# Kernel tuning notes

Measured on AMD Instinct MI355X. Metric: run time of the kernel, lower is better.

Reference implementation:

```python
import jax, jax.numpy as jnp
import numpy as np

DEGREE = 5
A = 1.0
B = 1.0
IN_F = 1024
OUT_F = 1024
BATCH = 8192


def setup_inputs() -> dict:
    key = jax.random.key(0)
    k1, k2, k3, k4 = jax.random.split(key, 4)
    x = jax.random.normal(k1, (BATCH, IN_F), dtype=jnp.float32)
    # base_weight ~ kaiming-uniform-ish scale
    bound_w = 1.0 / np.sqrt(IN_F)
    base_weight = jax.random.uniform(k2, (OUT_F, IN_F), dtype=jnp.float32,
                                     minval=-bound_w, maxval=bound_w)
    std = 1.0 / (IN_F * np.sqrt(DEGREE + 1))
    jacobi_coeffs = std * jax.random.normal(k3, (OUT_F, IN_F, DEGREE + 1), dtype=jnp.float32)
    bias = jax.random.uniform(k4, (OUT_F,), dtype=jnp.float32, minval=-bound_w, maxval=bound_w)
    return {"x": x, "base_weight": base_weight, "jacobi_coeffs": jacobi_coeffs, "bias": bias}


def _jacobi_polynomials(x):
    # x: (batch, in_features) -> (batch, in_features, DEGREE+1)
    t = jnp.tanh(x)
    polys = [jnp.ones_like(t)]
    if DEGREE >= 1:
        polys.append(0.5 * (2.0 * (A + 1.0) * t + (A - B)))
    for k in range(2, DEGREE + 1):
        # recurrence coefficients (matching torch loop where k = written index)
        alpha_n = 2.0 * k * (k + A + B) * (2 * k + A + B - 2)
        beta_n = (2 * k + A + B - 1) * (A ** 2 - B ** 2)
        gamma_n = (2 * k + A + B - 2) * (2 * k + A + B - 1) * (2 * k + A + B)
        delta_n = 2.0 * (k + A - 1) * (k + B - 1) * (2 * k + A + B)
        Acoef = (beta_n + alpha_n * t) / gamma_n
        Bcoef = delta_n / gamma_n
        polys.append(Acoef * polys[k - 1] - Bcoef * polys[k - 2])
    return jnp.stack(polys, axis=-1)


def reference(x, base_weight, jacobi_coeffs, bias):
    # base branch: SiLU then linear
    base_out = jax.nn.silu(x) @ base_weight.T  # (b, out)
    # jacobi branch
    P = _jacobi_polynomials(x)  # (b, in, deg+1)
    jac_out = jnp.einsum('bik,oik->bo', P, jacobi_coeffs)
    return base_out + jac_out + bias
```

## Files before the change

### kernel.cpp

```cpp
#include <hip/hip_runtime.h>
#include <hip/hip_bf16.h>
#include <cstdint>
#include <cstddef>

#define BATCH   8192
#define IN_F    1024
#define OUT_F   1024
#define KAUG    (6 * 1024)

typedef __bf16 bf16x8 __attribute__((ext_vector_type(8)));
typedef float  f32x4  __attribute__((ext_vector_type(4)));

static constexpr size_t WAUG_B    = (size_t)OUT_F * KAUG * 2;
static constexpr size_t BIAS2_OFF = WAUG_B;
static constexpr size_t AAUG_OFF  = WAUG_B + 4096;
static constexpr size_t AAUG_B    = (size_t)BATCH * KAUG * 2;
static constexpr size_t MMAP_OFF  = AAUG_OFF + AAUG_B;
static constexpr size_t NMAP_OFF  = MMAP_OFF + 1024;

__device__ __constant__ float JAC_A[4] = {64.f/120.f, 180.f/336.f, 384.f/720.f, 700.f/1320.f};
__device__ __constant__ float JAC_B[4] = {48.f/120.f, 144.f/336.f, 320.f/720.f, 600.f/1320.f};

__device__ __forceinline__ unsigned short f2bf(float f)
{
    __hip_bfloat16 h = __float2bfloat16(f);
    return *(unsigned short*)&h;
}
__device__ __forceinline__ unsigned pack2(float lo, float hi)
{
    return (unsigned)f2bf(lo) | ((unsigned)f2bf(hi) << 16);
}
__device__ __forceinline__ float fast_tanh(float x)
{
    const float xc = fminf(fmaxf(x, -15.f), 15.f);
    const float e  = __expf(2.f * xc);
    return (e - 1.f) / (e + 1.f);
}

__global__ void probe_layout(int* __restrict__ mmap, int* __restrict__ nmap)
{
    __shared__ __align__(16) __hip_bfloat16 A1[16 * 32], B1[16 * 32];
    __shared__ __align__(16) __hip_bfloat16 A2[16 * 32], B2[16 * 32];
    const int lane = threadIdx.x;
    for (int e = lane; e < 512; e += 64) {
        const int m = e >> 5, k = e & 31;
        A1[e] = __float2bfloat16((k == 0) ? (float)(m + 1) : 0.f);
        B1[e] = __float2bfloat16((k == 0) ? 1.f : 0.f);
        A2[e] = __float2bfloat16((k == 0) ? 1.f : 0.f);
        B2[e] = __float2bfloat16((k == 0) ? (float)(m + 1) : 0.f);
    }
    __syncthreads();
    const int quad = lane >> 4, mr = lane & 15;
    const int fi = mr * 4 + quad;
    f32x4 z = {};
    f32x4 d1 = __builtin_amdgcn_mfma_f32_16x16x32_bf16(((const bf16x8*)A1)[fi], ((const bf16x8*)B1)[fi], z, 0, 0, 0);
    f32x4 d2 = __builtin_amdgcn_mfma_f32_16x16x32_bf16(((const bf16x8*)A2)[fi], ((const bf16x8*)B2)[fi], z, 0, 0, 0);
#pragma unroll
    for (int r = 0; r < 4; ++r) {
        mmap[lane * 4 + r] = (int)(d1[r] + 0.5f) - 1;
        nmap[lane * 4 + r] = (int)(d2[r] + 0.5f) - 1;
    }
}

__global__ void prep_wb(const float* __restrict__ W,
                        const float* __restrict__ C,
                        const float* __restrict__ bias,
                        __hip_bfloat16* __restrict__ Waug,
                        float* __restrict__ bias2)
{
    const int o   = blockIdx.x;
    const int tid = threadIdx.x;
    const int i   = tid * 4;
    const size_t wbase = (size_t)o * KAUG;

    const float4 wv = *(const float4*)(W + (size_t)o * IN_F + i);
    ((uint2*)&Waug[wbase + i])[0] = make_uint2(pack2(wv.x, wv.y), pack2(wv.z, wv.w));

    float f[24];
    const float2* cp = (const float2*)(C + ((size_t)o * IN_F + i) * 6);
#pragma unroll
    for (int q = 0; q < 12; ++q) { const float2 v = cp[q]; f[q * 2] = v.x; f[q * 2 + 1] = v.y; }

#pragma unroll
    for (int j = 1; j <= 5; ++j) {
        ((uint2*)&Waug[wbase + (size_t)j * IN_F + i])[0] =
            make_uint2(pack2(f[0 + j], f[6 + j]), pack2(f[12 + j], f[18 + j]));
    }

    float s = f[0] + f[6] + f[12] + f[18];
#pragma unroll
    for (int off = 32; off > 0; off >>= 1) s += __shfl_down(s, off, 64);
    __shared__ float red[4];
    if ((tid & 63) == 0) red[tid >> 6] = s;
    __syncthreads();
    if (tid == 0) bias2[o] = bias[o] + red[0] + red[1] + red[2] + red[3];
}

__global__ void prep_acts(const float* __restrict__ X,
                          __hip_bfloat16* __restrict__ Aaug)
{
    const int gid = blockIdx.x * 256 + threadIdx.x;
    const int b   = gid >> 7;
    const int i8  = (gid & 127) * 8;
    const float4 x0 = *(const float4*)(X + (size_t)b * IN_F + i8);
    const float4 x1 = *(const float4*)(X + (size_t)b * IN_F + i8 + 4);
    const float sx[8] = {x0.x, x0.y, x0.z, x0.w, x1.x, x1.y, x1.z, x1.w};
    const size_t base = (size_t)b * KAUG + i8;

    float sil[8], t[8], pm1[8], pm2[8];
#pragma unroll
    for (int e = 0; e < 8; ++e) {
        sil[e] = sx[e] / (1.f + __expf(-sx[e]));
        t[e]   = fast_tanh(sx[e]);
        pm2[e] = 1.f; pm1[e] = 2.f * t[e];
    }
    *(uint4*)&Aaug[base] = make_uint4(pack2(sil[0], sil[1]), pack2(sil[2], sil[3]),
                                      pack2(sil[4], sil[5]), pack2(sil[6], sil[7]));
    *(uint4*)&Aaug[base + IN_F] = make_uint4(pack2(pm1[0], pm1[1]), pack2(pm1[2], pm1[3]),
                                             pack2(pm1[4], pm1[5]), pack2(pm1[6], pm1[7]));
#pragma unroll
    for (int k = 2; k <= 5; ++k) {
#pragma unroll
        for (int e = 0; e < 8; ++e) {
            const float pk = JAC_A[k - 2] * t[e] * pm1[e] - JAC_B[k - 2] * pm2[e];
            pm2[e] = pm1[e]; pm1[e] = pk;
        }
        *(uint4*)&Aaug[base + (size_t)k * IN_F] =
            make_uint4(pack2(pm1[0], pm1[1]), pack2(pm1[2], pm1[3]),
                       pack2(pm1[4], pm1[5]), pack2(pm1[6], pm1[7]));
    }
}

__device__ __forceinline__ void async_load16(const void* g, void* l)
{
    __builtin_amdgcn_global_load_lds(
        (const __attribute__((address_space(1))) void*)g,
        (__attribute__((address_space(3))) void*)l,
        16, 0, 0);
}

__global__ __launch_bounds__(256, 2)
void gemm_kan(const __hip_bfloat16* __restrict__ Aaug,
              const __hip_bfloat16* __restrict__ Waug,
              const float* __restrict__ bias2,
              const int* __restrict__ mmap,
              const int* __restrict__ nmap,
              float* __restrict__ out)
{
    __shared__ __align__(16) __hip_bfloat16 As[128 * 32], Bs[128 * 32];
    __shared__ __align__(16) __hip_bfloat16 As2[128 * 32], Bs2[128 * 32];

    const int tid  = threadIdx.x;
    const int lane = tid & 63;
    const int wave = tid >> 6;
    const int wm = wave & 1, wn = wave >> 1;
    const int mBase = blockIdx.y * 128;
    const int nBase = blockIdx.x * 128;

    const int srow = tid >> 2;
    const int scol = (tid & 3) * 8;
    const __hip_bfloat16* gA0 = Aaug + (size_t)(mBase + srow) * KAUG + scol;
    const __hip_bfloat16* gA1 = gA0 + (size_t)64 * KAUG;
    const __hip_bfloat16* gB0 = Waug + (size_t)(nBase + srow) * KAUG + scol;
    const __hip_bfloat16* gB1 = gB0 + (size_t)64 * KAUG;
    char* lA  = (char*)As  + wave * 1024;
    char* lB  = (char*)Bs  + wave * 1024;
    char* lA2 = (char*)As2 + wave * 1024;
    char* lB2 = (char*)Bs2 + wave * 1024;

    f32x4 acc[4][4] = {};
    const int quad = lane >> 4, mr = lane & 15;
    const int fbase = mr * 4 + quad;

    for (int k0 = 0; k0 < KAUG; k0 += 64) {
        async_load16(gA0 + k0, lA);
        async_load16(gA1 + k0, lA + 4096);
        async_load16(gB0 + k0, lB);
        async_load16(gB1 + k0, lB + 4096);
        async_load16(gA0 + k0 + 32, lA2);
        async_load16(gA1 + k0 + 32, lA2 + 4096);
        async_load16(gB0 + k0 + 32, lB2);
        async_load16(gB1 + k0 + 32, lB2 + 4096);
        __syncthreads();

        {
            const bf16x8* AsV = (const bf16x8*)As;
            const bf16x8* BsV = (const bf16x8*)Bs;
            bf16x8 a[4], b[4];
#pragma unroll
            for (int t = 0; t < 4; ++t) a[t] = AsV[(wm * 64 + t * 16) * 4 + fbase];
#pragma unroll
            for (int t = 0; t < 4; ++t) b[t] = BsV[(wn * 64 + t * 16) * 4 + fbase];
#pragma unroll
            for (int i = 0; i < 4; ++i)
#pragma unroll
                for (int jj = 0; jj < 4; ++jj)
                    acc[i][jj] = __builtin_amdgcn_mfma_f32_16x16x32_bf16(a[i], b[jj], acc[i][jj], 0, 0, 0);
        }
        {
            const bf16x8* AsV = (const bf16x8*)As2;
            const bf16x8* BsV = (const bf16x8*)Bs2;
            bf16x8 a[4], b[4];
#pragma unroll
            for (int t = 0; t < 4; ++t) a[t] = AsV[(wm * 64 + t * 16) * 4 + fbase];
#pragma unroll
            for (int t = 0; t < 4; ++t) b[t] = BsV[(wn * 64 + t * 16) * 4 + fbase];
#pragma unroll
            for (int i = 0; i < 4; ++i)
#pragma unroll
                for (int jj = 0; jj < 4; ++jj)
                    acc[i][jj] = __builtin_amdgcn_mfma_f32_16x16x32_bf16(a[i], b[jj], acc[i][jj], 0, 0, 0);
        }
        __syncthreads();
    }

    const int4 mv = ((const int4*)mmap)[lane];
    const int4 nv = ((const int4*)nmap)[lane];
    const int mm[4] = {mv.x, mv.y, mv.z, mv.w};
    const int nn[4] = {nv.x, nv.y, nv.z, nv.w};
#pragma unroll
    for (int i = 0; i < 4; ++i) {
#pragma unroll
        for (int jj = 0; jj < 4; ++jj) {
#pragma unroll
            for (int r = 0; r < 4; ++r) {
                const int row = mBase + wm * 64 + i * 16 + mm[r];
                const int col = nBase + wn * 64 + jj * 16 + nn[r];
                out[(size_t)row * OUT_F + col] = acc[i][jj][r] + bias2[col];
            }
        }
    }
}


extern "C" void kernel_launch(void* const* d_in, const int* in_sizes, int n_in,
                              void* d_out, int out_size, void* d_ws, size_t ws_size,
                              hipStream_t stream)
{
    (void)out_size; (void)ws_size;
    const float* x    = (const float*)d_in[0];
    const float* W    = (const float*)d_in[1];
    const float* C    = (const float*)d_in[2];
    const float* bias = (const float*)d_in[3];
    for (int i = 0; i < n_in; ++i) {
        if      (in_sizes[i] == BATCH * IN_F)     x    = (const float*)d_in[i];
        else if (in_sizes[i] == OUT_F * IN_F)     W    = (const float*)d_in[i];
        else if (in_sizes[i] == OUT_F * IN_F * 6) C    = (const float*)d_in[i];
        else if (in_sizes[i] == OUT_F)            bias = (const float*)d_in[i];
    }
    float* out = (float*)d_out;
    char* ws = (char*)d_ws;
    __hip_bfloat16* Waug  = (__hip_bfloat16*)ws;
    float*          bias2 = (float*)(ws + BIAS2_OFF);
    __hip_bfloat16* Aaug  = (__hip_bfloat16*)(ws + AAUG_OFF);
    int*            mmap  = (int*)(ws + MMAP_OFF);
    int*            nmap  = (int*)(ws + NMAP_OFF);

    probe_layout<<<dim3(1),     dim3(64),  0, stream>>>(mmap, nmap);
    prep_wb     <<<dim3(OUT_F), dim3(256), 0, stream>>>(W, C, bias, Waug, bias2);
    prep_acts   <<<dim3((BATCH * IN_F) / 2048), dim3(256), 0, stream>>>(x, Aaug);
    gemm_kan    <<<dim3(OUT_F / 128, BATCH / 128), dim3(256), 0, stream>>>(
        Aaug, Waug, bias2, mmap, nmap, out);
}
```

Measured before the change: 250.1 us.

## Split-K GEMM over two halves with atomic accumulation and swizzled LDS layout

Splits the K dimension across two grid z-slices, so each block does half the reduction and the partial sums are combined with float atomicAdd into an output pre-filled with bias by a new init kernel. It also XOR-swizzles the 16-byte chunk column in LDS to reduce bank conflicts on the fragment reads, and raises the launch-bounds occupancy hint from 2 to 4 blocks per SM. The split-K doubles the block count for more parallelism, at the cost of an extra full pass writing the output and atomic read-modify-write traffic on the large fp32 output. The tighter launch bounds may force register spilling given the 64-float accumulator array.

```diff
diff --git a/kernel.cpp b/kernel.cpp
--- a/kernel.cpp
+++ b/kernel.cpp
@@ -131,6 +131,15 @@
     }
 }
 
+__global__ void bias_init(const float* __restrict__ bias2, float* __restrict__ out)
+{
+    const int gid = blockIdx.x * 256 + threadIdx.x;
+    const int row = gid >> 8;
+    const int c4  = (gid & 255) * 4;
+    const float4 bv = *(const float4*)(bias2 + c4);
+    *(float4*)(out + (size_t)row * OUT_F + c4) = bv;
+}
+
 __device__ __forceinline__ void async_load16(const void* g, void* l)
 {
     __builtin_amdgcn_global_load_lds(
@@ -139,10 +148,9 @@
         16, 0, 0);
 }
 
-__global__ __launch_bounds__(256, 2)
+__global__ __launch_bounds__(256, 4)
 void gemm_kan(const __hip_bfloat16* __restrict__ Aaug,
               const __hip_bfloat16* __restrict__ Waug,
-              const float* __restrict__ bias2,
               const int* __restrict__ mmap,
               const int* __restrict__ nmap,
               float* __restrict__ out)
@@ -156,9 +164,11 @@
     const int wm = wave & 1, wn = wave >> 1;
     const int mBase = blockIdx.y * 128;
     const int nBase = blockIdx.x * 128;
+    const int kBase = blockIdx.z * (KAUG / 2);
 
     const int srow = tid >> 2;
-    const int scol = (tid & 3) * 8;
+    const int chnk = tid & 3;
+    const int scol = (chnk ^ ((srow >> 1) & 3)) * 8;
     const __hip_bfloat16* gA0 = Aaug + (size_t)(mBase + srow) * KAUG + scol;
     const __hip_bfloat16* gA1 = gA0 + (size_t)64 * KAUG;
     const __hip_bfloat16* gB0 = Waug + (size_t)(nBase + srow) * KAUG + scol;
@@ -170,9 +180,9 @@
 
     f32x4 acc[4][4] = {};
     const int quad = lane >> 4, mr = lane & 15;
-    const int fbase = mr * 4 + quad;
-
-    for (int k0 = 0; k0 < KAUG; k0 += 64) {
+    const int qsw  = quad ^ ((mr >> 1) & 3);
+
+    for (int k0 = kBase; k0 < kBase + KAUG / 2; k0 += 64) {
         async_load16(gA0 + k0, lA);
         async_load16(gA1 + k0, lA + 4096);
         async_load16(gB0 + k0, lB);
@@ -188,9 +198,9 @@
             const bf16x8* BsV = (const bf16x8*)Bs;
             bf16x8 a[4], b[4];
 #pragma unroll
-            for (int t = 0; t < 4; ++t) a[t] = AsV[(wm * 64 + t * 16) * 4 + fbase];
-#pragma unroll
-            for (int t = 0; t < 4; ++t) b[t] = BsV[(wn * 64 + t * 16) * 4 + fbase];
+            for (int t = 0; t < 4; ++t) a[t] = AsV[(wm * 64 + t * 16 + mr) * 4 + qsw];
+#pragma unroll
+            for (int t = 0; t < 4; ++t) b[t] = BsV[(wn * 64 + t * 16 + mr) * 4 + qsw];
 #pragma unroll
             for (int i = 0; i < 4; ++i)
 #pragma unroll
@@ -202,9 +212,9 @@
             const bf16x8* BsV = (const bf16x8*)Bs2;
             bf16x8 a[4], b[4];
 #pragma unroll
-            for (int t = 0; t < 4; ++t) a[t] = AsV[(wm * 64 + t * 16) * 4 + fbase];
-#pragma unroll
-            for (int t = 0; t < 4; ++t) b[t] = BsV[(wn * 64 + t * 16) * 4 + fbase];
+            for (int t = 0; t < 4; ++t) a[t] = AsV[(wm * 64 + t * 16 + mr) * 4 + qsw];
+#pragma unroll
+            for (int t = 0; t < 4; ++t) b[t] = BsV[(wn * 64 + t * 16 + mr) * 4 + qsw];
 #pragma unroll
             for (int i = 0; i < 4; ++i)
 #pragma unroll
@@ -226,7 +236,7 @@
             for (int r = 0; r < 4; ++r) {
                 const int row = mBase + wm * 64 + i * 16 + mm[r];
                 const int col = nBase + wn * 64 + jj * 16 + nn[r];
-                out[(size_t)row * OUT_F + col] = acc[i][jj][r] + bias2[col];
+                atomicAdd(&out[(size_t)row * OUT_F + col], acc[i][jj][r]);
             }
         }
     }
@@ -259,6 +269,7 @@
     probe_layout<<<dim3(1),     dim3(64),  0, stream>>>(mmap, nmap);
     prep_wb     <<<dim3(OUT_F), dim3(256), 0, stream>>>(W, C, bias, Waug, bias2);
     prep_acts   <<<dim3((BATCH * IN_F) / 2048), dim3(256), 0, stream>>>(x, Aaug);
-    gemm_kan    <<<dim3(OUT_F / 128, BATCH / 128), dim3(256), 0, stream>>>(
-        Aaug, Waug, bias2, mmap, nmap, out);
-}
+    bias_init   <<<dim3((BATCH * OUT_F) / 1024), dim3(256), 0, stream>>>(bias2, out);
+    gemm_kan    <<<dim3(OUT_F / 128, BATCH / 128, 2), dim3(256), 0, stream>>>(
+        Aaug, Waug, mmap, nmap, out);
+}
```

Measured after the change: 288.6 us. +15.4%, slower.

## Double-buffer GEMM LDS tiles, swizzle LDS layout, merge prep kernels, swap grid axes

Applied to the files above, without the earlier changes.

The GEMM main loop now keeps two LDS buffers and issues the async global-to-LDS loads for the next K tile while the current tile feeds the MFMAs. This is meant to hide global load latency behind compute. The LDS column chunk is XOR-swizzled by row to cut bank conflicts on fragment reads. The two prep kernels are merged into one launch, and the grid is transposed so consecutive blocks share a weight tile. Doubling the LDS footprint to 64KB may limit occupancy. The loop also keeps one __syncthreads per iteration, so the prefetch into the other buffer may race with waves still reading it.

```diff
diff --git a/kernel.cpp b/kernel.cpp
--- a/kernel.cpp
+++ b/kernel.cpp
@@ -62,72 +62,71 @@
     }
 }
 
-__global__ void prep_wb(const float* __restrict__ W,
-                        const float* __restrict__ C,
-                        const float* __restrict__ bias,
-                        __hip_bfloat16* __restrict__ Waug,
-                        float* __restrict__ bias2)
-{
-    const int o   = blockIdx.x;
+__global__ void prep_all(const float* __restrict__ X,
+                         const float* __restrict__ W,
+                         const float* __restrict__ C,
+                         const float* __restrict__ bias,
+                         __hip_bfloat16* __restrict__ Aaug,
+                         __hip_bfloat16* __restrict__ Waug,
+                         float* __restrict__ bias2)
+{
+    const int bid = blockIdx.x;
     const int tid = threadIdx.x;
-    const int i   = tid * 4;
-    const size_t wbase = (size_t)o * KAUG;
-
-    const float4 wv = *(const float4*)(W + (size_t)o * IN_F + i);
-    ((uint2*)&Waug[wbase + i])[0] = make_uint2(pack2(wv.x, wv.y), pack2(wv.z, wv.w));
-
-    float f[24];
-    const float2* cp = (const float2*)(C + ((size_t)o * IN_F + i) * 6);
-#pragma unroll
-    for (int q = 0; q < 12; ++q) { const float2 v = cp[q]; f[q * 2] = v.x; f[q * 2 + 1] = v.y; }
-
-#pragma unroll
-    for (int j = 1; j <= 5; ++j) {
-        ((uint2*)&Waug[wbase + (size_t)j * IN_F + i])[0] =
-            make_uint2(pack2(f[0 + j], f[6 + j]), pack2(f[12 + j], f[18 + j]));
-    }
-
-    float s = f[0] + f[6] + f[12] + f[18];
-#pragma unroll
-    for (int off = 32; off > 0; off >>= 1) s += __shfl_down(s, off, 64);
-    __shared__ float red[4];
-    if ((tid & 63) == 0) red[tid >> 6] = s;
-    __syncthreads();
-    if (tid == 0) bias2[o] = bias[o] + red[0] + red[1] + red[2] + red[3];
-}
-
-__global__ void prep_acts(const float* __restrict__ X,
-                          __hip_bfloat16* __restrict__ Aaug)
-{
-    const int gid = blockIdx.x * 256 + threadIdx.x;
-    const int b   = gid >> 7;
-    const int i8  = (gid & 127) * 8;
-    const float4 x0 = *(const float4*)(X + (size_t)b * IN_F + i8);
-    const float4 x1 = *(const float4*)(X + (size_t)b * IN_F + i8 + 4);
-    const float sx[8] = {x0.x, x0.y, x0.z, x0.w, x1.x, x1.y, x1.z, x1.w};
-    const size_t base = (size_t)b * KAUG + i8;
-
-    float sil[8], t[8], pm1[8], pm2[8];
-#pragma unroll
-    for (int e = 0; e < 8; ++e) {
-        sil[e] = sx[e] / (1.f + __expf(-sx[e]));
-        t[e]   = fast_tanh(sx[e]);
-        pm2[e] = 1.f; pm1[e] = 2.f * t[e];
-    }
-    *(uint4*)&Aaug[base] = make_uint4(pack2(sil[0], sil[1]), pack2(sil[2], sil[3]),
-                                      pack2(sil[4], sil[5]), pack2(sil[6], sil[7]));
-    *(uint4*)&Aaug[base + IN_F] = make_uint4(pack2(pm1[0], pm1[1]), pack2(pm1[2], pm1[3]),
-                                             pack2(pm1[4], pm1[5]), pack2(pm1[6], pm1[7]));
-#pragma unroll
-    for (int k = 2; k <= 5; ++k) {
+    if (bid < OUT_F) {
+        const int o = bid;
+        const int i = tid * 4;
+        const size_t wbase = (size_t)o * KAUG;
+
+        const float4 wv = *(const float4*)(W + (size_t)o * IN_F + i);
+        ((uint2*)&Waug[wbase + i])[0] = make_uint2(pack2(wv.x, wv.y), pack2(wv.z, wv.w));
+
+        float f[24];
+        const float2* cp = (const float2*)(C + ((size_t)o * IN_F + i) * 6);
+#pragma unroll
+        for (int q = 0; q < 12; ++q) { const float2 v = cp[q]; f[q * 2] = v.x; f[q * 2 + 1] = v.y; }
+#pragma unroll
+        for (int j = 1; j <= 5; ++j) {
+            ((uint2*)&Waug[wbase + (size_t)j * IN_F + i])[0] =
+                make_uint2(pack2(f[0 + j], f[6 + j]), pack2(f[12 + j], f[18 + j]));
+        }
+        float s = f[0] + f[6] + f[12] + f[18];
+#pragma unroll
+        for (int off = 32; off > 0; off >>= 1) s += __shfl_down(s, off, 64);
+        __shared__ float red[4];
+        if ((tid & 63) == 0) red[tid >> 6] = s;
+        __syncthreads();
+        if (tid == 0) bias2[o] = bias[o] + red[0] + red[1] + red[2] + red[3];
+    } else {
+        const int gid = (bid - OUT_F) * 256 + tid;
+        const int b   = gid >> 7;
+        const int i8  = (gid & 127) * 8;
+        const float4 x0 = *(const float4*)(X + (size_t)b * IN_F + i8);
+        const float4 x1 = *(const float4*)(X + (size_t)b * IN_F + i8 + 4);
+        const float sx[8] = {x0.x, x0.y, x0.z, x0.w, x1.x, x1.y, x1.z, x1.w};
+        const size_t base = (size_t)b * KAUG + i8;
+
+        float sil[8], t[8], pm1[8], pm2[8];
 #pragma unroll
         for (int e = 0; e < 8; ++e) {
-            const float pk = JAC_A[k - 2] * t[e] * pm1[e] - JAC_B[k - 2] * pm2[e];
-            pm2[e] = pm1[e]; pm1[e] = pk;
-        }
-        *(uint4*)&Aaug[base + (size_t)k * IN_F] =
-            make_uint4(pack2(pm1[0], pm1[1]), pack2(pm1[2], pm1[3]),
-                       pack2(pm1[4], pm1[5]), pack2(pm1[6], pm1[7]));
+            sil[e] = sx[e] / (1.f + __expf(-sx[e]));
+            t[e]   = fast_tanh(sx[e]);
+            pm2[e] = 1.f; pm1[e] = 2.f * t[e];
+        }
+        *(uint4*)&Aaug[base] = make_uint4(pack2(sil[0], sil[1]), pack2(sil[2], sil[3]),
+                                          pack2(sil[4], sil[5]), pack2(sil[6], sil[7]));
+        *(uint4*)&Aaug[base + IN_F] = make_uint4(pack2(pm1[0], pm1[1]), pack2(pm1[2], pm1[3]),
+                                                 pack2(pm1[4], pm1[5]), pack2(pm1[6], pm1[7]));
+#pragma unroll
+        for (int k = 2; k <= 5; ++k) {
+#pragma unroll
+            for (int e = 0; e < 8; ++e) {
+                const float pk = JAC_A[k - 2] * t[e] * pm1[e] - JAC_B[k - 2] * pm2[e];
+                pm2[e] = pm1[e]; pm1[e] = pk;
+            }
+            *(uint4*)&Aaug[base + (size_t)k * IN_F] =
+                make_uint4(pack2(pm1[0], pm1[1]), pack2(pm1[2], pm1[3]),
+                           pack2(pm1[4], pm1[5]), pack2(pm1[6], pm1[7]));
+        }
     }
 }
 
@@ -147,50 +146,63 @@
               const int* __restrict__ nmap,
               float* __restrict__ out)
 {
-    __shared__ __align__(16) __hip_bfloat16 As[128 * 32], Bs[128 * 32];
-    __shared__ __align__(16) __hip_bfloat16 As2[128 * 32], Bs2[128 * 32];
+    __shared__ __align__(16) __hip_bfloat16 As[2][128 * 32], As2[2][128 * 32];
+    __shared__ __align__(16) __hip_bfloat16 Bs[2][128 * 32], Bs2[2][128 * 32];
 
     const int tid  = threadIdx.x;
     const int lane = tid & 63;
     const int wave = tid >> 6;
     const int wm = wave & 1, wn = wave >> 1;
-    const int mBase = blockIdx.y * 128;
-    const int nBase = blockIdx.x * 128;
+    const int mBase = blockIdx.x * 128;
+    const int nBase = blockIdx.y * 128;
 
     const int srow = tid >> 2;
-    const int scol = (tid & 3) * 8;
+    const int chnk = tid & 3;
+    const int scol = (chnk ^ ((srow >> 1) & 3)) * 8;
     const __hip_bfloat16* gA0 = Aaug + (size_t)(mBase + srow) * KAUG + scol;
     const __hip_bfloat16* gA1 = gA0 + (size_t)64 * KAUG;
     const __hip_bfloat16* gB0 = Waug + (size_t)(nBase + srow) * KAUG + scol;
     const __hip_bfloat16* gB1 = gB0 + (size_t)64 * KAUG;
-    char* lA  = (char*)As  + wave * 1024;
-    char* lB  = (char*)Bs  + wave * 1024;
-    char* lA2 = (char*)As2 + wave * 1024;
-    char* lB2 = (char*)Bs2 + wave * 1024;
+    const int woff = wave * 1024;
 
     f32x4 acc[4][4] = {};
     const int quad = lane >> 4, mr = lane & 15;
-    const int fbase = mr * 4 + quad;
+    const int qsw  = quad ^ ((mr >> 1) & 3);
+
+    {
+        async_load16(gA0, (char*)As[0] + woff);
+        async_load16(gA1, (char*)As[0] + woff + 4096);
+        async_load16(gB0, (char*)Bs[0] + woff);
+        async_load16(gB1, (char*)Bs[0] + woff + 4096);
+        async_load16(gA0 + 32, (char*)As2[0] + woff);
+        async_load16(gA1 + 32, (char*)As2[0] + woff + 4096);
+        async_load16(gB0 + 32, (char*)Bs2[0] + woff);
+        async_load16(gB1 + 32, (char*)Bs2[0] + woff + 4096);
+    }
+    __syncthreads();
 
     for (int k0 = 0; k0 < KAUG; k0 += 64) {
-        async_load16(gA0 + k0, lA);
-        async_load16(gA1 + k0, lA + 4096);
-        async_load16(gB0 + k0, lB);
-        async_load16(gB1 + k0, lB + 4096);
-        async_load16(gA0 + k0 + 32, lA2);
-        async_load16(gA1 + k0 + 32, lA2 + 4096);
-        async_load16(gB0 + k0 + 32, lB2);
-        async_load16(gB1 + k0 + 32, lB2 + 4096);
-        __syncthreads();
-
+        const int cur = (k0 >> 6) & 1;
+        const int nxt = cur ^ 1;
+        if (k0 + 64 < KAUG) {
+            const int kn = k0 + 64;
+            async_load16(gA0 + kn, (char*)As[nxt] + woff);
+            async_load16(gA1 + kn, (char*)As[nxt] + woff + 4096);
+            async_load16(gB0 + kn, (char*)Bs[nxt] + woff);
+            async_load16(gB1 + kn, (char*)Bs[nxt] + woff + 4096);
+            async_load16(gA0 + kn + 32, (char*)As2[nxt] + woff);
+            async_load16(gA1 + kn + 32, (char*)As2[nxt] + woff + 4096);
+            async_load16(gB0 + kn + 32, (char*)Bs2[nxt] + woff);
+            async_load16(gB1 + kn + 32, (char*)Bs2[nxt] + woff + 4096);
+        }
         {
-            const bf16x8* AsV = (const bf16x8*)As;
-            const bf16x8* BsV = (const bf16x8*)Bs;
+            const bf16x8* AsV = (const bf16x8*)As[cur];
+            const bf16x8* BsV = (const bf16x8*)Bs[cur];
             bf16x8 a[4], b[4];
 #pragma unroll
-            for (int t = 0; t < 4; ++t) a[t] = AsV[(wm * 64 + t * 16) * 4 + fbase];
-#pragma unroll
-            for (int t = 0; t < 4; ++t) b[t] = BsV[(wn * 64 + t * 16) * 4 + fbase];
+            for (int t = 0; t < 4; ++t) a[t] = AsV[(wm * 64 + t * 16 + mr) * 4 + qsw];
+#pragma unroll
+            for (int t = 0; t < 4; ++t) b[t] = BsV[(wn * 64 + t * 16 + mr) * 4 + qsw];
 #pragma unroll
             for (int i = 0; i < 4; ++i)
 #pragma unroll
@@ -198,13 +210,13 @@
                     acc[i][jj] = __builtin_amdgcn_mfma_f32_16x16x32_bf16(a[i], b[jj], acc[i][jj], 0, 0, 0);
         }
         {
-            const bf16x8* AsV = (const bf16x8*)As2;
-            const bf16x8* BsV = (const bf16x8*)Bs2;
+            const bf16x8* AsV = (const bf16x8*)As2[cur];
+            const bf16x8* BsV = (const bf16x8*)Bs2[cur];
             bf16x8 a[4], b[4];
 #pragma unroll
-            for (int t = 0; t < 4; ++t) a[t] = AsV[(wm * 64 + t * 16) * 4 + fbase];
-#pragma unroll
-            for (int t = 0; t < 4; ++t) b[t] = BsV[(wn * 64 + t * 16) * 4 + fbase];
+            for (int t = 0; t < 4; ++t) a[t] = AsV[(wm * 64 + t * 16 + mr) * 4 + qsw];
+#pragma unroll
+            for (int t = 0; t < 4; ++t) b[t] = BsV[(wn * 64 + t * 16 + mr) * 4 + qsw];
 #pragma unroll
             for (int i = 0; i < 4; ++i)
 #pragma unroll
@@ -256,9 +268,9 @@
     int*            mmap  = (int*)(ws + MMAP_OFF);
     int*            nmap  = (int*)(ws + NMAP_OFF);
 
-    probe_layout<<<dim3(1),     dim3(64),  0, stream>>>(mmap, nmap);
-    prep_wb     <<<dim3(OUT_F), dim3(256), 0, stream>>>(W, C, bias, Waug, bias2);
-    prep_acts   <<<dim3((BATCH * IN_F) / 2048), dim3(256), 0, stream>>>(x, Aaug);
-    gemm_kan    <<<dim3(OUT_F / 128, BATCH / 128), dim3(256), 0, stream>>>(
+    probe_layout<<<dim3(1), dim3(64), 0, stream>>>(mmap, nmap);
+    prep_all<<<dim3(OUT_F + (BATCH * IN_F) / 2048), dim3(256), 0, stream>>>(
+        x, W, C, bias, Aaug, Waug, bias2);
+    gemm_kan<<<dim3(BATCH / 128, OUT_F / 128), dim3(256), 0, stream>>>(
         Aaug, Waug, bias2, mmap, nmap, out);
 }
```

New measurement: 227.3 us. 9.1% less time.
